# Optimization experiments

Measured on AMD Instinct MI355X. Metric: run time of the kernel, lower is better.

Reference implementation:

```python
import jax, jax.numpy as jnp
import numpy as np

B, LATENT, FEAT, SEQ = 64, 512, 256, 512
EPS = 1e-5


def setup_inputs() -> dict:
    key = jax.random.key(0)
    ks = jax.random.split(key, 14)
    rn = lambda k, shape, s=0.05: jax.random.normal(k, shape, jnp.float32) * s
    return {
        "h0": rn(ks[0], (1, B, LATENT), 1.0),
        "c0": rn(ks[1], (1, B, LATENT), 1.0),
        "seq_len": SEQ,
        # LSTMCell params (torch layout: [4*hidden, in] / [4*hidden, hidden])
        "W_ih": rn(ks[2], (4 * LATENT, FEAT)),
        "b_ih": rn(ks[3], (4 * LATENT,)),
        "W_hh": rn(ks[4], (4 * LATENT, LATENT)),
        "b_hh": rn(ks[5], (4 * LATENT,)),
        # dense_dec1: Linear(latent -> n_features)
        "W_dense": rn(ks[6], (FEAT, LATENT)),
        "b_dense": rn(ks[7], (FEAT,)),
        # ConvTranspose1d weights, torch layout [C_in, C_out, k]
        "w_dc1": rn(ks[8], (FEAT, FEAT, 3)),
        "b_dc1": rn(ks[9], (FEAT,)),
        "w_dc2": rn(ks[10], (FEAT, FEAT, 3)),
        "b_dc2": rn(ks[11], (FEAT,)),
        # BatchNorm1d affine params
        "gamma": jnp.ones((FEAT,), jnp.float32),
        "beta": jnp.zeros((FEAT,), jnp.float32),
    }


def _deconv1d(x, w, b):
    """torch ConvTranspose1d(k=3, stride=2, padding=1, output_padding=1): L -> 2L.
    x: [B, C, L], w: [C_in, C_out, k] (torch layout)."""
    wf = jnp.flip(w, -1).transpose(1, 0, 2)  # [C_out, C_in, k]
    y = jax.lax.conv_general_dilated(
        x, wf, window_strides=(1,), padding=[(1, 2)], lhs_dilation=(2,),
        dimension_numbers=("NCH", "OIH", "NCH"))
    return y + b[None, :, None]


def reference(h0, c0, seq_len, W_ih, b_ih, W_hh, b_hh, W_dense, b_dense,
              w_dc1, b_dc1, w_dc2, b_dc2, gamma, beta):
    h, c = h0[0], c0[0]                       # squeeze(0): [B, latent]
    x0 = h @ W_dense.T + b_dense              # initial dense_dec1(h_0[0])

    def step(carry, _):
        h, c, x_in = carry
        gates = x_in @ W_ih.T + b_ih + h @ W_hh.T + b_hh   # [B, 4*latent]
        i, f, g, o = jnp.split(gates, 4, axis=-1)
        i, f, o = jax.nn.sigmoid(i), jax.nn.sigmoid(f), jax.nn.sigmoid(o)
        g = jnp.tanh(g)
        c2 = f * c + i * g
        h2 = o * jnp.tanh(c2)
        x2 = h2 @ W_dense.T + b_dense
        return (h2, c2, x2), x2

    _, xs = jax.lax.scan(step, (h, c, x0), None, length=seq_len)  # [T, B, F]
    x = xs.transpose(1, 2, 0)                  # cat+view+swapaxes -> [B, F, T]

    x = _deconv1d(x, w_dc1, b_dc1)             # [B, F, 2T]
    x = jax.nn.relu(x)
    # BatchNorm1d in training mode: batch stats over (N, L) per channel
    mean = x.mean(axis=(0, 2), keepdims=True)
    var = x.var(axis=(0, 2), keepdims=True)
    x = (x - mean) / jnp.sqrt(var + EPS) * gamma[None, :, None] + beta[None, :, None]
    x = _deconv1d(x, w_dc2, b_dc2)             # [B, F, 4T]
    return x.swapaxes(1, 2)                    # [B, 4T, F]
```

## Files before the change

kernel.cpp:

```cpp
#include <hip/hip_runtime.h>
#include <hip/hip_bf16.h>
#include <math.h>

#define LB __launch_bounds__(256)

namespace {
constexpr int BB  = 64;
constexpr int LAT = 512;
constexpr int FE  = 256;
constexpr int TT  = 512;
constexpr int G4  = 2048;
constexpr int LO1 = 1024;
constexpr int LO2 = 2048;
constexpr int Y1S = 1025;
constexpr float EPSV = 1e-5f;

constexpr size_t OFF_WT   = 0;
constexpr size_t OFF_WTB  = OFF_WT  + (size_t)G4 * LAT;
constexpr size_t OFF_BC   = OFF_WTB + (size_t)G4 * LAT / 2;
constexpr size_t OFF_HX   = OFF_BC  + G4;
constexpr size_t OFF_A    = OFF_HX  + (size_t)4 * 2 * 8192;
constexpr size_t OFF_CBV  = OFF_A   + (size_t)3 * LAT * FE;
constexpr size_t OFF_GSUM = OFF_CBV + 3 * FE;
constexpr size_t OFF_GSQ  = OFF_GSUM + FE;
constexpr size_t OFF_BNSC = OFF_GSQ  + FE;
constexpr size_t OFF_BNSH = OFF_BNSC + FE;
constexpr size_t OFF_BSH  = OFF_BNSH + FE;
constexpr size_t OFF_BP1  = OFF_BSH + 3 * FE;
constexpr size_t OFF_BP2  = OFF_BP1 + (size_t)3*16*16*64*8/2;
constexpr size_t OFF_HSB  = OFF_BP2 + (size_t)3*8*16*64*8/2;
constexpr size_t OFF_Y1P  = OFF_HSB + (size_t)513*64*512/2;
}

typedef __attribute__((ext_vector_type(8))) short s8v;
typedef __attribute__((ext_vector_type(4))) float f4v;
typedef __attribute__((ext_vector_type(4))) unsigned u4v;

__device__ __forceinline__ void store_wt_u(unsigned* p, unsigned v) {
    asm volatile("global_store_dword %0, %1, off sc0 sc1" :: "v"(p), "v"(v) : "memory");
}
__device__ __forceinline__ unsigned pack_pair(float h, int ep) {
    return ((__float_as_uint(h) + 0x8000u) & 0xFFFF0000u) | (unsigned)ep;
}
__device__ __forceinline__ unsigned short f2bf(float h) {
    return (unsigned short)((__float_as_uint(h) + 0x8000u) >> 16);
}
__device__ __forceinline__ float sigmoid_fast(float x) {
    return 1.f / (1.f + __expf(-x));
}
__device__ __forceinline__ float tanh_fast(float x) {
    float e = __expf(2.f * fminf(x, 15.f));
    return (e - 1.f) / (e + 1.f);
}

__global__ LB void k_build_wcomb(const float* __restrict__ Wd, const float* __restrict__ Wih,
                                 const float* __restrict__ Whh, float* __restrict__ Wt,
                                 unsigned short* __restrict__ Wtb) {
    int idx = blockIdx.x * 256 + threadIdx.x;
    int k = idx & (LAT - 1);
    int g = idx >> 9;
    float acc = Whh[(size_t)g * LAT + k];
#pragma unroll 4
    for (int c = 0; c < FE; ++c)
        acc = fmaf(Wd[(size_t)c * LAT + k], Wih[(size_t)g * FE + c], acc);
    Wt[(size_t)g * LAT + k] = acc;
    Wtb[(size_t)g * LAT + k] = f2bf(acc);
}

__global__ LB void k_build_bcomb(const float* __restrict__ Wih, const float* __restrict__ bih,
                                 const float* __restrict__ bhh, const float* __restrict__ bd,
                                 float* __restrict__ bc) {
    int g = blockIdx.x * 256 + threadIdx.x;
    float acc = bih[g] + bhh[g];
#pragma unroll 4
    for (int c = 0; c < FE; ++c) acc = fmaf(Wih[(size_t)g * FE + c], bd[c], acc);
    bc[g] = acc;
}

__global__ LB void k_build_A(const float* __restrict__ Wd, const float* __restrict__ w1,
                             float* __restrict__ A) {
    int idx = blockIdx.x * 256 + threadIdx.x;
    int co = idx & 255, ki = (idx >> 8) & 511, tap = idx >> 17;
    float acc = 0.f;
#pragma unroll 4
    for (int c = 0; c < FE; ++c)
        acc = fmaf(Wd[(size_t)c * LAT + ki], w1[((size_t)c * FE + co) * 3 + tap], acc);
    A[((size_t)tap * LAT + ki) * FE + co] = acc;
}

__global__ LB void k_build_cb(const float* __restrict__ bd, const float* __restrict__ w1,
                              float* __restrict__ cbv) {
    int tap = blockIdx.x, co = threadIdx.x;
    float acc = 0.f;
#pragma unroll 4
    for (int c = 0; c < FE; ++c) acc = fmaf(bd[c], w1[((size_t)c * FE + co) * 3 + tap], acc);
    cbv[tap * FE + co] = acc;
}

__global__ LB void k_bpack1(const float* __restrict__ A, unsigned short* __restrict__ Bp1) {
    int idx = blockIdx.x * 256 + threadIdx.x;
    int j = idx & 7, lane = (idx >> 3) & 63, ct = (idx >> 9) & 15;
    int ks = (idx >> 13) & 15, tap = idx >> 17;
    int k = ks * 32 + (lane >> 4) * 8 + j;
    int co = ct * 16 + (lane & 15);
    Bp1[idx] = f2bf(A[((size_t)tap * LAT + k) * FE + co]);
}

__global__ LB void k_init_misc(float* __restrict__ gsum, float* __restrict__ gsq,
                               unsigned* __restrict__ Hx) {
    int idx = blockIdx.x * 256 + threadIdx.x;
    Hx[idx] = 0u;
    if (idx < FE) { gsum[idx] = 0.f; gsq[idx] = 0.f; }
}

__global__ LB void k_init_pads(unsigned short* __restrict__ Hsb,
                               unsigned short* __restrict__ Y1p) {
    int idx = blockIdx.x * 256 + threadIdx.x;
    if (idx < 32768) {
        Hsb[(size_t)512 * BB * LAT + idx] = 0;
    } else {
        int j = idx - 32768;
        int b = j >> 8, co = j & 255;
        Y1p[((size_t)b * Y1S + 1024) * FE + co] = 0;
    }
}

#define LDG16(o, p)                                                             \
    asm volatile(                                                               \
        "global_load_dword %0,  %16, off sc0 sc1\n\t"                           \
        "global_load_dword %1,  %16, off offset:64 sc0 sc1\n\t"                 \
        "global_load_dword %2,  %16, off offset:128 sc0 sc1\n\t"                \
        "global_load_dword %3,  %16, off offset:192 sc0 sc1\n\t"                \
        "global_load_dword %4,  %16, off offset:256 sc0 sc1\n\t"                \
        "global_load_dword %5,  %16, off offset:320 sc0 sc1\n\t"                \
        "global_load_dword %6,  %16, off offset:384 sc0 sc1\n\t"                \
        "global_load_dword %7,  %16, off offset:448 sc0 sc1\n\t"                \
        "global_load_dword %8,  %16, off offset:512 sc0 sc1\n\t"                \
        "global_load_dword %9,  %16, off offset:576 sc0 sc1\n\t"                \
        "global_load_dword %10, %16, off offset:640 sc0 sc1\n\t"                \
        "global_load_dword %11, %16, off offset:704 sc0 sc1\n\t"                \
        "global_load_dword %12, %16, off offset:768 sc0 sc1\n\t"                \
        "global_load_dword %13, %16, off offset:832 sc0 sc1\n\t"                \
        "global_load_dword %14, %16, off offset:896 sc0 sc1\n\t"                \
        "global_load_dword %15, %16, off offset:960 sc0 sc1"                    \
        : "=&v"(u[(o) + 0]), "=&v"(u[(o) + 1]), "=&v"(u[(o) + 2]),              \
          "=&v"(u[(o) + 3]), "=&v"(u[(o) + 4]), "=&v"(u[(o) + 5]),              \
          "=&v"(u[(o) + 6]), "=&v"(u[(o) + 7]), "=&v"(u[(o) + 8]),              \
          "=&v"(u[(o) + 9]), "=&v"(u[(o) + 10]), "=&v"(u[(o) + 11]),            \
          "=&v"(u[(o) + 12]), "=&v"(u[(o) + 13]), "=&v"(u[(o) + 14]),           \
          "=&v"(u[(o) + 15])                                                    \
        : "v"(p))

__global__ __launch_bounds__(256, 1) void k_lstm_grp2(
    const unsigned short* __restrict__ Wtb, const float* __restrict__ bc,
    const float* __restrict__ h0, const float* __restrict__ c0,
    unsigned* __restrict__ Hx, unsigned short* __restrict__ Hsb)
{
    __shared__ unsigned A_lds[16 * 264];
    __shared__ float gbuf[4][16][16];
    const int w = blockIdx.x, tid = threadIdx.x;
    const int g = w >> 6, jt = w & 63;
    const int b = tid & 15, kq = tid >> 4;
    const int wv = tid >> 6, lane = tid & 63;
    const int n = wv & 1, kh = wv >> 1;
    unsigned* buf0 = Hx + (size_t)g * 2 * 8192;
    unsigned* buf1 = buf0 + 8192;

    s8v Bf[8];
    {
        int c = 16 * n + (lane & 15);
        int gg = (c >> 3) * LAT + jt * 8 + (c & 7);
        const unsigned short* bp = Wtb + (size_t)gg * LAT + kh * 256 + (lane >> 4) * 8;
#pragma unroll
        for (int ks = 0; ks < 8; ++ks)
            Bf[ks] = *(const s8v*)(bp + ks * 32);
    }

    float creg = 0.f, bs0 = 0.f, bs1 = 0.f, bs2 = 0.f, bs3 = 0.f;
    if (tid < 128) {
        int p = tid >> 4, b3 = tid & 15;
        int j = jt * 8 + p, bg = g * 16 + b3;
        creg = c0[(size_t)bg * LAT + j];
        bs0 = bc[0 * LAT + j];
        bs1 = bc[1 * LAT + j];
        bs2 = bc[2 * LAT + j];
        bs3 = bc[3 * LAT + j];
        store_wt_u(&buf0[j * 16 + b3], pack_pair(h0[(size_t)bg * LAT + j], 1));
    }
    __syncthreads();

    for (int t = 0; t < TT; ++t) {
        const unsigned* __restrict__ cur = (t & 1) ? buf1 : buf0;
        unsigned* __restrict__ nxt = (t & 1) ? buf0 : buf1;
        const int ep = t + 1;

        unsigned u[32];
        const unsigned* pb = cur + kq * 512 + b;
        for (;;) {
            LDG16(0, pb);
            LDG16(16, pb + 256);
            asm volatile("s_waitcnt vmcnt(0)" ::: "memory");
            __builtin_amdgcn_sched_barrier(0);
            int mn = 0x7fffffff;
#pragma unroll
            for (int i = 0; i < 32; ++i) mn = min(mn, (int)(u[i] & 0xFFFFu));
            if (__all(mn >= ep)) break;
            __builtin_amdgcn_s_sleep(2);
        }

        {
            unsigned* dst = A_lds + b * 264 + kq * 16;
#pragma unroll
            for (int q4 = 0; q4 < 4; ++q4) {
                u4v v = (u4v){
                    (u[q4*8+0] >> 16) | (u[q4*8+1] & 0xFFFF0000u),
                    (u[q4*8+2] >> 16) | (u[q4*8+3] & 0xFFFF0000u),
                    (u[q4*8+4] >> 16) | (u[q4*8+5] & 0xFFFF0000u),
                    (u[q4*8+6] >> 16) | (u[q4*8+7] & 0xFFFF0000u) };
                *(u4v*)(dst + q4 * 4) = v;
            }
        }
        __syncthreads();

        f4v acc = (f4v){0.f, 0.f, 0.f, 0.f};
#pragma unroll
        for (int ks = 0; ks < 8; ++ks) {
            const unsigned* ap = A_lds + (lane & 15) * 264 + kh * 128 + ks * 16
                               + (lane >> 4) * 4;
            u4v av = *(const u4v*)ap;
            acc = __builtin_amdgcn_mfma_f32_16x16x32_bf16(
                      __builtin_bit_cast(s8v, av), Bf[ks], acc, 0, 0, 0);
        }
#pragma unroll
        for (int q = 0; q < 4; ++q)
            gbuf[wv][(lane >> 4) * 4 + q][lane & 15] = acc[q];
        __syncthreads();

        if (tid < 128) {
            int p = tid >> 4, b3 = tid & 15;
            int j = jt * 8 + p, bg = g * 16 + b3;
            float gi = gbuf[0][b3][p]      + gbuf[2][b3][p];
            float gf = gbuf[0][b3][8 + p]  + gbuf[2][b3][8 + p];
            float gg2 = gbuf[1][b3][p]     + gbuf[3][b3][p];
            float go = gbuf[1][b3][8 + p]  + gbuf[3][b3][8 + p];
            gi += bs0; gf += bs1; gg2 += bs2; go += bs3;
            float ii = sigmoid_fast(gi);
            float ff = sigmoid_fast(gf);
            float tg = tanh_fast(gg2);
            float oo = sigmoid_fast(go);
            creg = ff * creg + ii * tg;
            float hv = oo * tanh_fast(creg);
            unsigned pk = pack_pair(hv, t + 2);
            store_wt_u(&nxt[j * 16 + b3], pk);
            Hsb[((size_t)t * BB + bg) * LAT + j] = (unsigned short)(pk >> 16);
        }
        __syncthreads();
    }
}

__global__ LB void k_mfma_dc1(const unsigned short* __restrict__ Hsb,
                              const unsigned short* __restrict__ Bp1,
                              const float* __restrict__ cbv, const float* __restrict__ b1,
                              unsigned short* __restrict__ Y1p,
                              float* __restrict__ gsum, float* __restrict__ gsq) {
    __shared__ float s_sum[64], s_sq[64];
    int blk = blockIdx.x;
    int bm = blk >> 2, bn = blk & 3;
    int tid = threadIdx.x, wv = tid >> 6, lane = tid & 63;
    if (tid < 64) { s_sum[tid] = 0.f; s_sq[tid] = 0.f; }
    __syncthreads();
    int m0 = bm * 64 + wv * 16;
    const unsigned short* pa = Hsb + (size_t)(m0 + (lane & 15)) * LAT + (lane >> 4) * 8;
    const unsigned short* pas = pa + (size_t)64 * LAT;
    f4v acce[4], acco[4];
#pragma unroll
    for (int c = 0; c < 4; ++c) { acce[c] = (f4v){0.f,0.f,0.f,0.f}; acco[c] = (f4v){0.f,0.f,0.f,0.f}; }
    for (int ks = 0; ks < 16; ++ks) {
        s8v av = *(const s8v*)(pa + ks * 32);
        s8v as = *(const s8v*)(pas + ks * 32);
#pragma unroll
        for (int c = 0; c < 4; ++c) {
            int ct = bn * 4 + c;
            const size_t fb = ((size_t)ks * 16 + ct) * 64 + lane;
            s8v bf1 = *(const s8v*)(Bp1 + (((size_t)1 * 16 * 16 * 64) + fb) * 8);
            s8v bf2 = *(const s8v*)(Bp1 + (((size_t)2 * 16 * 16 * 64) + fb) * 8);
            s8v bf0 = *(const s8v*)(Bp1 + (fb) * 8);
            acce[c] = __builtin_amdgcn_mfma_f32_16x16x32_bf16(av, bf1, acce[c], 0, 0, 0);
            acco[c] = __builtin_amdgcn_mfma_f32_16x16x32_bf16(av, bf2, acco[c], 0, 0, 0);
            acco[c] = __builtin_amdgcn_mfma_f32_16x16x32_bf16(as, bf0, acco[c], 0, 0, 0);
        }
    }
#pragma unroll
    for (int c = 0; c < 4; ++c) {
        int col = bn * 64 + c * 16 + (lane & 15);
        float be = cbv[FE + col] + b1[col];
        float bo = cbv[2 * FE + col] + b1[col] + cbv[col];
        float c0v = cbv[col];
        float ps = 0.f, pq = 0.f;
#pragma unroll
        for (int q = 0; q < 4; ++q) {
            int r = m0 + (lane >> 4) * 4 + q;
            int i = r >> 6, b = r & 63;
            float ve = acce[c][q] + be;
            float vo = acco[c][q] + bo;
            if (i == TT - 1) vo -= c0v;
            ve = fmaxf(ve, 0.f);
            vo = fmaxf(vo, 0.f);
            size_t base = ((size_t)b * Y1S + 2 * i) * FE + col;
            Y1p[base] = f2bf(ve);
            Y1p[base + FE] = f2bf(vo);
            ps += ve + vo;
            pq += ve * ve + vo * vo;
        }
        atomicAdd(&s_sum[c * 16 + (lane & 15)], ps);
        atomicAdd(&s_sq[c * 16 + (lane & 15)], pq);
    }
    __syncthreads();
    if (tid < 64) {
        atomicAdd(&gsum[bn * 64 + tid], s_sum[tid]);
        atomicAdd(&gsq[bn * 64 + tid], s_sq[tid]);
    }
}

__global__ LB void k_bnfin(const float* __restrict__ gsum, const float* __restrict__ gsq,
                           const float* __restrict__ gamma, const float* __restrict__ beta,
                           float* __restrict__ bnsc, float* __restrict__ bnsh) {
    int co = threadIdx.x;
    float n = (float)(BB * LO1);
    float m = gsum[co] / n;
    float v = gsq[co] / n - m * m;
    float sc = gamma[co] / sqrtf(v + EPSV);
    bnsc[co] = sc;
    bnsh[co] = beta[co] - m * sc;
}

__global__ LB void k_fold_bias2(const float* __restrict__ bnsh, const float* __restrict__ w2,
                                float* __restrict__ bsh) {
    int tap = blockIdx.x, co = threadIdx.x;
    float acc = 0.f;
#pragma unroll 4
    for (int c = 0; c < FE; ++c) acc = fmaf(bnsh[c], w2[((size_t)c * FE + co) * 3 + tap], acc);
    bsh[tap * FE + co] = acc;
}

__global__ LB void k_bpack2(const float* __restrict__ bnsc, const float* __restrict__ w2,
                            unsigned short* __restrict__ Bp2) {
    int idx = blockIdx.x * 256 + threadIdx.x;
    int j = idx & 7, lane = (idx >> 3) & 63, ct = (idx >> 9) & 15;
    int ks = (idx >> 13) & 7, tap = idx >> 16;
    int ci = ks * 32 + (lane >> 4) * 8 + j;
    int co = ct * 16 + (lane & 15);
    Bp2[idx] = f2bf(bnsc[ci] * w2[((size_t)ci * FE + co) * 3 + tap]);
}

__global__ LB void k_mfma_dc2(const unsigned short* __restrict__ Y1p,
                              const unsigned short* __restrict__ Bp2,
                              const float* __restrict__ b2, const float* __restrict__ bsh,
                              float* __restrict__ out) {
    int blk = blockIdx.x;
    int b = blk >> 6, lt = (blk >> 2) & 15, bn = blk & 3;
    int tid = threadIdx.x, wv = tid >> 6, lane = tid & 63;
    int l0 = lt * 64 + wv * 16;
    const unsigned short* pa = Y1p + ((size_t)b * Y1S + l0 + (lane & 15)) * FE + (lane >> 4) * 8;
    const unsigned short* pas = pa + FE;
    f4v acce[4], acco[4];
#pragma unroll
    for (int c = 0; c < 4; ++c) { acce[c] = (f4v){0.f,0.f,0.f,0.f}; acco[c] = (f4v){0.f,0.f,0.f,0.f}; }
    for (int ks = 0; ks < 8; ++ks) {
        s8v av = *(const s8v*)(pa + ks * 32);
        s8v as = *(const s8v*)(pas + ks * 32);
#pragma unroll
        for (int c = 0; c < 4; ++c) {
            int ct = bn * 4 + c;
            const size_t fb = ((size_t)ks * 16 + ct) * 64 + lane;
            s8v bf1 = *(const s8v*)(Bp2 + (((size_t)1 * 8 * 16 * 64) + fb) * 8);
            s8v bf2 = *(const s8v*)(Bp2 + (((size_t)2 * 8 * 16 * 64) + fb) * 8);
            s8v bf0 = *(const s8v*)(Bp2 + (fb) * 8);
            acce[c] = __builtin_amdgcn_mfma_f32_16x16x32_bf16(av, bf1, acce[c], 0, 0, 0);
            acco[c] = __builtin_amdgcn_mfma_f32_16x16x32_bf16(av, bf2, acco[c], 0, 0, 0);
            acco[c] = __builtin_amdgcn_mfma_f32_16x16x32_bf16(as, bf0, acco[c], 0, 0, 0);
        }
    }
#pragma unroll
    for (int c = 0; c < 4; ++c) {
        int col = bn * 64 + c * 16 + (lane & 15);
        float be = b2[col] + bsh[FE + col];
        float bo = b2[col] + bsh[2 * FE + col] + bsh[col];
        float s0 = bsh[col];
#pragma unroll
        for (int q = 0; q < 4; ++q) {
            int l = l0 + (lane >> 4) * 4 + q;
            float ve = acce[c][q] + be;
            float vo = acco[c][q] + bo;
            if (l == LO1 - 1) vo -= s0;
            size_t base = ((size_t)b * LO2 + 2 * l) * FE + col;
            out[base] = ve;
            out[base + FE] = vo;
        }
    }
}

extern "C" void kernel_launch(void* const* d_in, const int* in_sizes, int n_in,
                              void* d_out, int out_size, void* d_ws, size_t ws_size,
                              hipStream_t stream) {
    const float* h0    = (const float*)d_in[0];
    const float* c0    = (const float*)d_in[1];
    const float* Wih   = (const float*)d_in[3];
    const float* bih   = (const float*)d_in[4];
    const float* Whh   = (const float*)d_in[5];
    const float* bhh   = (const float*)d_in[6];
    const float* Wd    = (const float*)d_in[7];
    const float* bd    = (const float*)d_in[8];
    const float* w1    = (const float*)d_in[9];
    const float* b1    = (const float*)d_in[10];
    const float* w2    = (const float*)d_in[11];
    const float* b2    = (const float*)d_in[12];
    const float* gamma = (const float*)d_in[13];
    const float* beta  = (const float*)d_in[14];

    float* ws   = (float*)d_ws;
    float* Wt   = ws + OFF_WT;
    unsigned short* Wtb = (unsigned short*)(ws + OFF_WTB);
    float* bc   = ws + OFF_BC;
    unsigned* Hx  = (unsigned*)(ws + OFF_HX);
    float* A    = ws + OFF_A;
    float* cbv  = ws + OFF_CBV;
    float* gsum = ws + OFF_GSUM;
    float* gsq  = ws + OFF_GSQ;
    float* bnsc = ws + OFF_BNSC;
    float* bnsh = ws + OFF_BNSH;
    float* bsh  = ws + OFF_BSH;
    unsigned short* Bp1 = (unsigned short*)(ws + OFF_BP1);
    unsigned short* Bp2 = (unsigned short*)(ws + OFF_BP2);
    unsigned short* Hsb = (unsigned short*)(ws + OFF_HSB);
    unsigned short* Y1p = (unsigned short*)(ws + OFF_Y1P);
    float* out  = (float*)d_out;

    k_build_wcomb<<<4096, 256, 0, stream>>>(Wd, Wih, Whh, Wt, Wtb);
    k_build_bcomb<<<8, 256, 0, stream>>>(Wih, bih, bhh, bd, bc);
    k_build_A<<<1536, 256, 0, stream>>>(Wd, w1, A);
    k_build_cb<<<3, 256, 0, stream>>>(bd, w1, cbv);
    k_bpack1<<<1536, 256, 0, stream>>>(A, Bp1);
    k_init_misc<<<256, 256, 0, stream>>>(gsum, gsq, Hx);
    k_init_pads<<<192, 256, 0, stream>>>(Hsb, Y1p);

    {
        const unsigned short* a0 = Wtb;  const float* a1 = bc;
        const float* a2 = h0;  const float* a3 = c0;
        unsigned* a4 = Hx; unsigned short* a5 = Hsb;
        void* args[] = { (void*)&a0, (void*)&a1, (void*)&a2, (void*)&a3,
                         (void*)&a4, (void*)&a5 };
        hipLaunchCooperativeKernel((const void*)k_lstm_grp2, dim3(256), dim3(256),
                                   args, 0, stream);
    }

    k_mfma_dc1<<<2048, 256, 0, stream>>>(Hsb, Bp1, cbv, b1, Y1p, gsum, gsq);
    k_bnfin<<<1, 256, 0, stream>>>(gsum, gsq, gamma, beta, bnsc, bnsh);
    k_fold_bias2<<<3, 256, 0, stream>>>(bnsh, w2, bsh);
    k_bpack2<<<768, 256, 0, stream>>>(bnsc, w2, Bp2);
    k_mfma_dc2<<<4096, 256, 0, stream>>>(Y1p, Bp2, b2, bsh, out);
}
```

Baseline: 1.812 ms.

## Compute LSTM gates in registers with lane shuffles, removing the LDS gate reduction

The LSTM step kernel now has two waves each run the full K=512 MFMA chain (16 k-steps) over a gate-interleaved column layout, so each lane holds one gate for one hidden unit. The cell update is then done with cross-lane shuffles, which removes the gbuf LDS round trip, one __syncthreads per timestep and the split-K partial-sum addition. The A tile row stride is padded from 264 to 268 to reduce LDS bank conflicts, and the unused fp32 combined-weight buffer is dropped. In exchange only half of the waves do MFMA work, so each active wave carries a longer serial MFMA chain per step.

```diff
diff --git a/kernel.cpp b/kernel.cpp
--- a/kernel.cpp
+++ b/kernel.cpp
@@ -15,8 +15,7 @@
 constexpr int Y1S = 1025;
 constexpr float EPSV = 1e-5f;
 
-constexpr size_t OFF_WT   = 0;
-constexpr size_t OFF_WTB  = OFF_WT  + (size_t)G4 * LAT;
+constexpr size_t OFF_WTB  = 0;
 constexpr size_t OFF_BC   = OFF_WTB + (size_t)G4 * LAT / 2;
 constexpr size_t OFF_HX   = OFF_BC  + G4;
 constexpr size_t OFF_A    = OFF_HX  + (size_t)4 * 2 * 8192;
@@ -54,7 +53,7 @@
 }
 
 __global__ LB void k_build_wcomb(const float* __restrict__ Wd, const float* __restrict__ Wih,
-                                 const float* __restrict__ Whh, float* __restrict__ Wt,
+                                 const float* __restrict__ Whh,
                                  unsigned short* __restrict__ Wtb) {
     int idx = blockIdx.x * 256 + threadIdx.x;
     int k = idx & (LAT - 1);
@@ -63,7 +62,6 @@
 #pragma unroll 4
     for (int c = 0; c < FE; ++c)
         acc = fmaf(Wd[(size_t)c * LAT + k], Wih[(size_t)g * FE + c], acc);
-    Wt[(size_t)g * LAT + k] = acc;
     Wtb[(size_t)g * LAT + k] = f2bf(acc);
 }
 
@@ -151,40 +149,42 @@
           "=&v"(u[(o) + 15])                                                    \
         : "v"(p))
 
-__global__ __launch_bounds__(256, 1) void k_lstm_grp2(
+__global__ __launch_bounds__(256, 1) void k_lstm_grp3(
     const unsigned short* __restrict__ Wtb, const float* __restrict__ bc,
     const float* __restrict__ h0, const float* __restrict__ c0,
     unsigned* __restrict__ Hx, unsigned short* __restrict__ Hsb)
 {
-    __shared__ unsigned A_lds[16 * 264];
-    __shared__ float gbuf[4][16][16];
+    __shared__ unsigned A_lds[16 * 268];
     const int w = blockIdx.x, tid = threadIdx.x;
     const int g = w >> 6, jt = w & 63;
     const int b = tid & 15, kq = tid >> 4;
     const int wv = tid >> 6, lane = tid & 63;
-    const int n = wv & 1, kh = wv >> 1;
     unsigned* buf0 = Hx + (size_t)g * 2 * 8192;
     unsigned* buf1 = buf0 + 8192;
 
-    s8v Bf[8];
-    {
-        int c = 16 * n + (lane & 15);
-        int gg = (c >> 3) * LAT + jt * 8 + (c & 7);
-        const unsigned short* bp = Wtb + (size_t)gg * LAT + kh * 256 + (lane >> 4) * 8;
-#pragma unroll
-        for (int ks = 0; ks < 8; ++ks)
+    s8v Bf[16];
+    float bs = 0.f, creg[4] = {0.f, 0.f, 0.f, 0.f};
+    int jlane = 0, slane = 0;
+    if (wv < 2) {
+        int c = lane & 15;
+        slane = c & 3;
+        jlane = jt * 8 + wv * 4 + (c >> 2);
+        int gg = slane * LAT + jlane;
+        const unsigned short* bp = Wtb + (size_t)gg * LAT + (lane >> 4) * 8;
+#pragma unroll
+        for (int ks = 0; ks < 16; ++ks)
             Bf[ks] = *(const s8v*)(bp + ks * 32);
-    }
-
-    float creg = 0.f, bs0 = 0.f, bs1 = 0.f, bs2 = 0.f, bs3 = 0.f;
+        bs = bc[slane * LAT + jlane];
+#pragma unroll
+        for (int q = 0; q < 4; ++q) {
+            int bg = g * 16 + (lane >> 4) * 4 + q;
+            creg[q] = c0[(size_t)bg * LAT + jlane];
+        }
+    }
+
     if (tid < 128) {
         int p = tid >> 4, b3 = tid & 15;
         int j = jt * 8 + p, bg = g * 16 + b3;
-        creg = c0[(size_t)bg * LAT + j];
-        bs0 = bc[0 * LAT + j];
-        bs1 = bc[1 * LAT + j];
-        bs2 = bc[2 * LAT + j];
-        bs3 = bc[3 * LAT + j];
         store_wt_u(&buf0[j * 16 + b3], pack_pair(h0[(size_t)bg * LAT + j], 1));
     }
     __syncthreads();
@@ -209,7 +209,7 @@
         }
 
         {
-            unsigned* dst = A_lds + b * 264 + kq * 16;
+            unsigned* dst = A_lds + b * 268 + kq * 16;
 #pragma unroll
             for (int q4 = 0; q4 < 4; ++q4) {
                 u4v v = (u4v){
@@ -222,37 +222,37 @@
         }
         __syncthreads();
 
-        f4v acc = (f4v){0.f, 0.f, 0.f, 0.f};
-#pragma unroll
-        for (int ks = 0; ks < 8; ++ks) {
-            const unsigned* ap = A_lds + (lane & 15) * 264 + kh * 128 + ks * 16
-                               + (lane >> 4) * 4;
-            u4v av = *(const u4v*)ap;
-            acc = __builtin_amdgcn_mfma_f32_16x16x32_bf16(
-                      __builtin_bit_cast(s8v, av), Bf[ks], acc, 0, 0, 0);
-        }
-#pragma unroll
-        for (int q = 0; q < 4; ++q)
-            gbuf[wv][(lane >> 4) * 4 + q][lane & 15] = acc[q];
-        __syncthreads();
-
-        if (tid < 128) {
-            int p = tid >> 4, b3 = tid & 15;
-            int j = jt * 8 + p, bg = g * 16 + b3;
-            float gi = gbuf[0][b3][p]      + gbuf[2][b3][p];
-            float gf = gbuf[0][b3][8 + p]  + gbuf[2][b3][8 + p];
-            float gg2 = gbuf[1][b3][p]     + gbuf[3][b3][p];
-            float go = gbuf[1][b3][8 + p]  + gbuf[3][b3][8 + p];
-            gi += bs0; gf += bs1; gg2 += bs2; go += bs3;
-            float ii = sigmoid_fast(gi);
-            float ff = sigmoid_fast(gf);
-            float tg = tanh_fast(gg2);
-            float oo = sigmoid_fast(go);
-            creg = ff * creg + ii * tg;
-            float hv = oo * tanh_fast(creg);
-            unsigned pk = pack_pair(hv, t + 2);
-            store_wt_u(&nxt[j * 16 + b3], pk);
-            Hsb[((size_t)t * BB + bg) * LAT + j] = (unsigned short)(pk >> 16);
+        if (wv < 2) {
+            f4v acc = (f4v){0.f, 0.f, 0.f, 0.f};
+#pragma unroll
+            for (int ks = 0; ks < 16; ++ks) {
+                const unsigned* ap = A_lds + (lane & 15) * 268 + ks * 16
+                                   + (lane >> 4) * 4;
+                u4v av = *(const u4v*)ap;
+                acc = __builtin_amdgcn_mfma_f32_16x16x32_bf16(
+                          __builtin_bit_cast(s8v, av), Bf[ks], acc, 0, 0, 0);
+            }
+#pragma unroll
+            for (int q = 0; q < 4; ++q) {
+                float v = acc[q] + bs;
+                float e = (slane == 2) ? tanh_fast(v) : sigmoid_fast(v);
+                float tg  = __shfl_xor(e, 2);
+                float p1  = e * tg;
+                float p1x = __shfl_xor(p1, 1);
+                float c2  = fmaf(e, creg[q], p1x);
+                creg[q]   = c2;
+                float t2  = tanh_fast(c2);
+                float t2x = __shfl_xor(t2, 2);
+                float hv  = e * t2x;
+                if (slane == 3) {
+                    int bl = (lane >> 4) * 4 + q;
+                    int bg = g * 16 + bl;
+                    unsigned pk = pack_pair(hv, t + 2);
+                    store_wt_u(&nxt[jlane * 16 + bl], pk);
+                    Hsb[((size_t)t * BB + bg) * LAT + jlane] =
+                        (unsigned short)(pk >> 16);
+                }
+            }
         }
         __syncthreads();
     }
@@ -419,7 +419,6 @@
     const float* beta  = (const float*)d_in[14];
 
     float* ws   = (float*)d_ws;
-    float* Wt   = ws + OFF_WT;
     unsigned short* Wtb = (unsigned short*)(ws + OFF_WTB);
     float* bc   = ws + OFF_BC;
     unsigned* Hx  = (unsigned*)(ws + OFF_HX);
@@ -436,7 +435,7 @@
     unsigned short* Y1p = (unsigned short*)(ws + OFF_Y1P);
     float* out  = (float*)d_out;
 
-    k_build_wcomb<<<4096, 256, 0, stream>>>(Wd, Wih, Whh, Wt, Wtb);
+    k_build_wcomb<<<4096, 256, 0, stream>>>(Wd, Wih, Whh, Wtb);
     k_build_bcomb<<<8, 256, 0, stream>>>(Wih, bih, bhh, bd, bc);
     k_build_A<<<1536, 256, 0, stream>>>(Wd, w1, A);
     k_build_cb<<<3, 256, 0, stream>>>(bd, w1, cbv);
@@ -450,7 +449,7 @@
         unsigned* a4 = Hx; unsigned short* a5 = Hsb;
         void* args[] = { (void*)&a0, (void*)&a1, (void*)&a2, (void*)&a3,
                          (void*)&a4, (void*)&a5 };
-        hipLaunchCooperativeKernel((const void*)k_lstm_grp2, dim3(256), dim3(256),
+        hipLaunchCooperativeKernel((const void*)k_lstm_grp3, dim3(256), dim3(256),
                                    args, 0, stream);
     }
 
```

Result: slower. 2.348 ms (+29.6%).
